# Kernel optimization log

Hardware: AMD Instinct MI355X
Metric: run time of the kernel (lower is better)

## Reference

```python
import jax, jax.numpy as jnp
import numpy as np

N, E = 50000, 800000
IN, OUT, ED = 64, 128, 16
L_CONV, CLS, L_CLS = 4, 256, 2
NUM_MOLS = 2000
BN_INV = 1.0 / np.sqrt(1.0 + 1e-5).astype(np.float32)  # BN eval: running_mean=0, running_var=1


def leaky(v):
    return jnp.where(v > 0, v, 0.01 * v)


def gine_conv(x, src, dst, edge_attr, eW, eb, W, b, gamma, beta):
    # PyG GINEConv (eps=0): nn(x + sum_j relu(x_j + lin_e(edge_attr)))
    e = edge_attr @ eW + eb                       # [E, d_in]
    msg = jax.nn.relu(x[src] + e)                 # [E, d_in]
    agg = jax.ops.segment_sum(msg, dst, num_segments=N)  # [N, d_in]
    h = (x + agg) @ W + b                         # [N, OUT]
    h = gamma * (h * BN_INV) + beta               # BatchNorm1d (eval)
    return leaky(h)                               # LeakyReLU inside nn (Dropout=identity)


def setup_inputs() -> dict:
    key = jax.random.key(0)
    ks = jax.random.split(key, 24)
    s = 0.05
    inp = {
        "x": jax.random.normal(ks[0], (N, IN), jnp.float32),
        "edge_index": jax.random.randint(ks[1], (2, E), 0, N, jnp.int32),
        "edge_attr": jax.random.normal(ks[2], (E, ED), jnp.float32),
        "batch": jnp.sort(jax.random.randint(ks[3], (N,), 0, NUM_MOLS, jnp.int32)),
        "conv1_W": jax.random.normal(ks[4], (IN, OUT), jnp.float32) * s,
        "conv1_b": jnp.zeros((OUT,), jnp.float32),
        "conv1_gamma": jnp.ones((OUT,), jnp.float32),
        "conv1_beta": jnp.zeros((OUT,), jnp.float32),
        "conv1_eW": jax.random.normal(ks[5], (ED, IN), jnp.float32) * s,
        "conv1_eb": jnp.zeros((IN,), jnp.float32),
        "conv_W": jax.random.normal(ks[6], (L_CONV, OUT, OUT), jnp.float32) * s,
        "conv_b": jnp.zeros((L_CONV, OUT), jnp.float32),
        "conv_gamma": jnp.ones((L_CONV, OUT), jnp.float32),
        "conv_beta": jnp.zeros((L_CONV, OUT), jnp.float32),
        "conv_eW": jax.random.normal(ks[7], (L_CONV, ED, OUT), jnp.float32) * s,
        "conv_eb": jnp.zeros((L_CONV, OUT), jnp.float32),
        "cls1_W": jax.random.normal(ks[8], (OUT * (L_CONV + 1), CLS), jnp.float32) * s,
        "cls1_b": jnp.zeros((CLS,), jnp.float32),
        "cls_W": jax.random.normal(ks[9], (L_CLS, CLS, CLS), jnp.float32) * s,
        "cls_b": jnp.zeros((L_CLS, CLS), jnp.float32),
        "final_W": jax.random.normal(ks[10], (CLS, 1), jnp.float32) * s,
        "final_b": jnp.zeros((1,), jnp.float32),
    }
    return inp


def reference(x, edge_index, edge_attr, batch,
              conv1_W, conv1_b, conv1_gamma, conv1_beta, conv1_eW, conv1_eb,
              conv_W, conv_b, conv_gamma, conv_beta, conv_eW, conv_eb,
              cls1_W, cls1_b, cls_W, cls_b, final_W, final_b):
    src, dst = edge_index[0], edge_index[1]
    h = gine_conv(x, src, dst, edge_attr, conv1_eW, conv1_eb,
                  conv1_W, conv1_b, conv1_gamma, conv1_beta)
    h = leaky(h)  # outer LeakyReLU in forward (note: conv1 output not in hs)
    hs = []
    for i in range(conv_W.shape[0]):
        h = gine_conv(h, src, dst, edge_attr, conv_eW[i], conv_eb[i],
                      conv_W[i], conv_b[i], conv_gamma[i], conv_beta[i])
        h = leaky(h)
        hs.append(h)
    h_pool = jax.ops.segment_sum(h, batch, num_segments=NUM_MOLS)  # global_add_pool
    h_pool_nodes = h_pool[batch]  # repeat_interleave by per-mol counts (batch sorted)
    h = jnp.concatenate(hs + [h_pool_nodes], axis=1)  # [N, OUT*(L_CONV+1)]
    h = h @ cls1_W + cls1_b  # no activation after classifier1 (as in source)
    for i in range(cls_W.shape[0]):
        h = leaky(h @ cls_W[i] + cls_b[i])
    return jax.nn.sigmoid(h @ final_W + final_b)  # [N, 1]
```

## Files before the change

### kernel.cpp

```cpp
#include <hip/hip_runtime.h>
#include <hip/hip_bf16.h>
#include <math.h>

#define N_NODES 50000
#define N_EDGES 800000
#define N_MOLS  2000
#define EPB     128

static constexpr float BN_INV_F = 0.9999950000374997f;

enum { ACT_NONE = 0, ACT_LEAKY = 1, ACT_BN_DL = 2 };

typedef float f32x4 __attribute__((ext_vector_type(4)));
typedef short bf16x8 __attribute__((ext_vector_type(8)));

static __device__ __forceinline__ float b2f(short s) {
    unsigned u = ((unsigned)(unsigned short)s) << 16;
    return __builtin_bit_cast(float, u);
}
static __device__ __forceinline__ short f2bs(float v) {
    return __builtin_bit_cast(short, __float2bfloat16(v));
}


__global__ void hist_kernel(const int* __restrict__ ei, int* __restrict__ cnt) {
    int e = blockIdx.x * 256 + threadIdx.x;
    if (e < N_EDGES) atomicAdd(&cnt[ei[N_EDGES + e]], 1);
}

__global__ __launch_bounds__(1024) void scan1_kernel(const int* __restrict__ cnt,
                                                     int* __restrict__ incl,
                                                     int* __restrict__ bsum) {
    __shared__ int sd[1024];
    int i = blockIdx.x * 1024 + threadIdx.x;
    int v = (i < N_NODES) ? cnt[i] : 0;
    sd[threadIdx.x] = v;
    __syncthreads();
    for (int off = 1; off < 1024; off <<= 1) {
        int t = (threadIdx.x >= off) ? sd[threadIdx.x - off] : 0;
        __syncthreads();
        sd[threadIdx.x] += t;
        __syncthreads();
    }
    incl[i] = sd[threadIdx.x];
    if (threadIdx.x == 1023) bsum[blockIdx.x] = sd[1023];
}

__global__ void scan2_kernel(const int* __restrict__ bsum, int* __restrict__ bex, int nblk) {
    if (threadIdx.x == 0) {
        int run = 0;
        for (int b = 0; b < nblk; ++b) { bex[b] = run; run += bsum[b]; }
    }
}

__global__ __launch_bounds__(1024) void scan3_kernel(const int* __restrict__ cnt,
                                                     const int* __restrict__ incl,
                                                     const int* __restrict__ bex,
                                                     int* __restrict__ cursor) {
    int i = blockIdx.x * 1024 + threadIdx.x;
    if (i < N_NODES) cursor[i] = bex[blockIdx.x] + incl[i] - cnt[i];
}

__global__ void scatter_kernel(const int* __restrict__ ei, int* __restrict__ cursor,
                               const float* __restrict__ ea,
                               int* __restrict__ srcs, int* __restrict__ dsts,
                               __hip_bfloat16* __restrict__ eas) {
    int e = blockIdx.x * 256 + threadIdx.x;
    if (e < N_EDGES) {
        int d = ei[N_EDGES + e];
        int pos = atomicAdd(&cursor[d], 1);
        srcs[pos] = ei[e];
        dsts[pos] = d;
        const f32x4* s4 = (const f32x4*)(ea + (size_t)e * 16);
        f32x4 a0 = s4[0], a1 = s4[1], a2 = s4[2], a3 = s4[3];
        bf16x8 lo, hi;
#pragma unroll
        for (int j = 0; j < 4; ++j) {
            lo[j] = f2bs(a0[j]); lo[4 + j] = f2bs(a1[j]);
            hi[j] = f2bs(a2[j]); hi[4 + j] = f2bs(a3[j]);
        }
        bf16x8* d8 = (bf16x8*)(eas + (size_t)pos * 16);
        d8[0] = lo; d8[1] = hi;
    }
}


__global__ __launch_bounds__(256) void cvt_all_kernel(
        const float* __restrict__ c1W, const float* __restrict__ cW,
        const float* __restrict__ cls1W, const float* __restrict__ clsW,
        const float* __restrict__ c1eW, const float* __restrict__ ceW,
        __hip_bfloat16* __restrict__ wt1, __hip_bfloat16* __restrict__ wtc,
        __hip_bfloat16* __restrict__ wtcls1, __hip_bfloat16* __restrict__ wtcls,
        __hip_bfloat16* __restrict__ ewt1, __hip_bfloat16* __restrict__ ewtc) {
    int o = blockIdx.x * 256 + threadIdx.x;
    auto cvt = [](const float* s, __hip_bfloat16* d, int K, int Nc, int off) {
        int n = off / K, k = off - n * K;
        d[off] = __float2bfloat16(s[(size_t)k * Nc + n]);
    };
    if (o < 8192) cvt(c1W, wt1, 64, 128, o);
    else if (o < 73728)  { int s = o - 8192;   int i = s >> 14, off = s & 16383;
        cvt(cW + i * 16384, wtc + i * 16384, 128, 128, off); }
    else if (o < 237568) cvt(cls1W, wtcls1, 640, 256, o - 73728);
    else if (o < 368640) { int s = o - 237568; int i = s >> 16, off = s & 65535;
        cvt(clsW + i * 65536, wtcls + i * 65536, 256, 256, off); }
    else if (o < 369664) cvt(c1eW, ewt1, 16, 64, o - 368640);
    else if (o < 377856) { int s = o - 369664; int i = s >> 11, off = s & 2047;
        cvt(ceW + i * 2048, ewtc + i * 2048, 16, 128, off); }
}


template<int D, bool F32IN>
__global__ __launch_bounds__(256) void edge_mfma_kernel(
        const void* __restrict__ hin_, int ld,
        const __hip_bfloat16* __restrict__ eas,
        const int* __restrict__ srcs,
        const int* __restrict__ dsts,
        const __hip_bfloat16* __restrict__ eWt,
        const float* __restrict__ eb,
        float* __restrict__ t32) {
    constexpr int SP = D + 4;
    constexpr int NCT = D / 16;
    constexpr int GROUPS = 256 / D;
    constexpr int EPG = EPB / GROUPS;
    __shared__ __hip_bfloat16 e_lds[EPB * SP];
    const int tid = threadIdx.x;
    const int wid = tid >> 6, lane = tid & 63;
    const int lrow = lane & 15;
    const int lkg = lane >> 4;
    const bool hiK = lkg >= 2;
    const int lko = (lkg & 1) * 8;
    const int p0 = blockIdx.x * EPB;

    bf16x8 bfrag[NCT];
#pragma unroll
    for (int ct = 0; ct < NCT; ++ct) {
        bf16x8 bv = *reinterpret_cast<const bf16x8*>(&eWt[(ct * 16 + lrow) * 16 + lko]);
        if (hiK) bv = (bf16x8){0, 0, 0, 0, 0, 0, 0, 0};
        bfrag[ct] = bv;
    }
#pragma unroll
    for (int et = 0; et < 2; ++et) {
        const int erow = (wid * 2 + et) * 16;
        bf16x8 av = *reinterpret_cast<const bf16x8*>(
            &eas[(size_t)(p0 + erow + lrow) * 16 + lko]);
        if (hiK) av = (bf16x8){0, 0, 0, 0, 0, 0, 0, 0};
        const int r0 = erow + lkg * 4;
#pragma unroll
        for (int ct = 0; ct < NCT; ++ct) {
            f32x4 c = (f32x4){0.f, 0.f, 0.f, 0.f};
            c = __builtin_amdgcn_mfma_f32_16x16x32_bf16(av, bfrag[ct], c, 0, 0, 0);
            const int col = ct * 16 + lrow;
            const float bi = eb[col];
#pragma unroll
            for (int r = 0; r < 4; ++r)
                e_lds[(r0 + r) * SP + col] = __float2bfloat16(c[r] + bi);
        }
    }
    __syncthreads();

    const float* hf = (const float*)hin_;
    const __hip_bfloat16* hb = (const __hip_bfloat16*)hin_;
    const int g = tid / D;
    const int f = tid - g * D;
    const int q0 = g * EPG;
    int cur = dsts[p0 + q0];
    float acc = 0.f;
    for (int q = q0; q < q0 + EPG; q += 8) {
        int s[8], d[8];
#pragma unroll
        for (int j = 0; j < 8; ++j) { s[j] = srcs[p0 + q + j]; d[j] = dsts[p0 + q + j]; }
        float h[8];
#pragma unroll
        for (int j = 0; j < 8; ++j)
            h[j] = F32IN ? hf[(size_t)s[j] * ld + f]
                         : __bfloat162float(hb[(size_t)s[j] * ld + f]);
        float e[8];
#pragma unroll
        for (int j = 0; j < 8; ++j)
            e[j] = __bfloat162float(e_lds[(q + j) * SP + f]);
#pragma unroll
        for (int j = 0; j < 8; ++j) {
            if (d[j] != cur) {
                atomicAdd(&t32[(size_t)cur * D + f], acc);
                acc = 0.f; cur = d[j];
            }
            acc += fmaxf(h[j] + e[j], 0.f);
        }
    }
    atomicAdd(&t32[(size_t)cur * D + f], acc);
}


template<int DIN, int DOUT, int WR, int WC, int MT, int NT, int ACT, int SELF>
__global__ __launch_bounds__(256) void mfma_lin_kernel(
        const void* __restrict__ A_, int lda,
        const float* __restrict__ t32,
        const __hip_bfloat16* __restrict__ Wt,
        const float* __restrict__ bias,
        const float* __restrict__ gamma,
        const float* __restrict__ beta,
        __hip_bfloat16* __restrict__ C, int ldc) {
    constexpr int BROWS = WR * MT * 16;
    constexpr int NKS = DIN / 32;
    static_assert(WC * NT * 16 == DOUT, "cols");
    static_assert(WR * WC == 4, "waves");
    const int wid = threadIdx.x >> 6, lane = threadIdx.x & 63;
    const int wr = wid / WC, wc = wid % WC;
    const int row_base = blockIdx.x * BROWS + wr * MT * 16;
    const int col0 = wc * NT * 16;
    const int lrow = lane & 15;
    const int lk = (lane >> 4) * 8;

    f32x4 acc[MT][NT];
#pragma unroll
    for (int i = 0; i < MT; ++i)
#pragma unroll
        for (int j = 0; j < NT; ++j) acc[i][j] = (f32x4){0.f, 0.f, 0.f, 0.f};

    for (int ks = 0; ks < NKS; ++ks) {
        const int kc = ks * 32 + lk;
        bf16x8 b[NT];
#pragma unroll
        for (int nt = 0; nt < NT; ++nt)
            b[nt] = *reinterpret_cast<const bf16x8*>(
                &Wt[(size_t)(col0 + nt * 16 + lrow) * DIN + kc]);
#pragma unroll
        for (int mt = 0; mt < MT; ++mt) {
            int arow = row_base + mt * 16 + lrow;
            arow = arow < N_NODES ? arow : N_NODES - 1;
            bf16x8 a;
            if constexpr (SELF == 0) {
                a = *reinterpret_cast<const bf16x8*>(
                    &((const __hip_bfloat16*)A_)[(size_t)arow * lda + kc]);
            } else {
                f32x4 t0 = *(const f32x4*)&t32[(size_t)arow * DIN + kc];
                f32x4 t1 = *(const f32x4*)&t32[(size_t)arow * DIN + kc + 4];
                if constexpr (SELF == 1) {
                    f32x4 h0 = *(const f32x4*)&((const float*)A_)[(size_t)arow * lda + kc];
                    f32x4 h1 = *(const f32x4*)&((const float*)A_)[(size_t)arow * lda + kc + 4];
#pragma unroll
                    for (int j = 0; j < 4; ++j) {
                        a[j]     = f2bs(t0[j] + h0[j]);
                        a[4 + j] = f2bs(t1[j] + h1[j]);
                    }
                } else {
                    bf16x8 hv = *reinterpret_cast<const bf16x8*>(
                        &((const __hip_bfloat16*)A_)[(size_t)arow * lda + kc]);
#pragma unroll
                    for (int j = 0; j < 4; ++j) {
                        a[j]     = f2bs(t0[j] + b2f(hv[j]));
                        a[4 + j] = f2bs(t1[j] + b2f(hv[4 + j]));
                    }
                }
            }
#pragma unroll
            for (int nt = 0; nt < NT; ++nt)
                acc[mt][nt] = __builtin_amdgcn_mfma_f32_16x16x32_bf16(
                    a, b[nt], acc[mt][nt], 0, 0, 0);
        }
    }

#pragma unroll
    for (int mt = 0; mt < MT; ++mt) {
        int r0 = row_base + mt * 16 + (lane >> 4) * 4;
#pragma unroll
        for (int nt = 0; nt < NT; ++nt) {
            int c = col0 + nt * 16 + lrow;
            float bi = bias[c];
            float ga = (ACT == ACT_BN_DL) ? gamma[c] : 0.f;
            float be = (ACT == ACT_BN_DL) ? beta[c] : 0.f;
#pragma unroll
            for (int r = 0; r < 4; ++r) {
                int row = r0 + r;
                if (row < N_NODES) {
                    float v = acc[mt][nt][r] + bi;
                    if (ACT == ACT_BN_DL) {
                        v = ga * (v * BN_INV_F) + be;
                        v = v > 0.f ? v : 1e-4f * v;
                    } else if (ACT == ACT_LEAKY) {
                        v = v > 0.f ? v : 0.01f * v;
                    }
                    C[(size_t)row * ldc + c] = __float2bfloat16(v);
                }
            }
        }
    }
}


__global__ void pool_add_kernel(const __hip_bfloat16* __restrict__ concat,
                                const int* __restrict__ batch,
                                float* __restrict__ pool) {
    int idx = blockIdx.x * 256 + threadIdx.x;
    if (idx >= N_NODES * 128) return;
    int n = idx >> 7, f = idx & 127;
    atomicAdd(&pool[batch[n] * 128 + f],
              __bfloat162float(concat[(size_t)n * 640 + 384 + f]));
}

__global__ void pool_gather_kernel(__hip_bfloat16* __restrict__ concat,
                                   const int* __restrict__ batch,
                                   const float* __restrict__ pool) {
    int idx = blockIdx.x * 256 + threadIdx.x;
    if (idx >= N_NODES * 128) return;
    int n = idx >> 7, f = idx & 127;
    concat[(size_t)n * 640 + 512 + f] = __float2bfloat16(pool[batch[n] * 128 + f]);
}


__global__ __launch_bounds__(256) void final_kernel(const __hip_bfloat16* __restrict__ A,
                                                    const float* __restrict__ fW,
                                                    const float* __restrict__ fb,
                                                    float* __restrict__ out) {
    int wave = threadIdx.x >> 6;
    int lane = threadIdx.x & 63;
    int row = blockIdx.x * 4 + wave;
    const __hip_bfloat16* ar = A + (size_t)row * 256;
    float p = 0.f;
#pragma unroll
    for (int i = 0; i < 4; ++i) {
        int k = lane + i * 64;
        p += __bfloat162float(ar[k]) * fW[k];
    }
#pragma unroll
    for (int off = 32; off >= 1; off >>= 1) p += __shfl_xor(p, off, 64);
    if (lane == 0) out[row] = 1.f / (1.f + expf(-(p + fb[0])));
}


extern "C" void kernel_launch(void* const* d_in, const int* in_sizes, int n_in,
                              void* d_out, int out_size, void* d_ws, size_t ws_size,
                              hipStream_t stream) {
    const float* x     = (const float*)d_in[0];
    const int*   ei    = (const int*)d_in[1];
    const float* ea    = (const float*)d_in[2];
    const int*   batch = (const int*)d_in[3];
    const float* c1W   = (const float*)d_in[4];
    const float* c1b   = (const float*)d_in[5];
    const float* c1g   = (const float*)d_in[6];
    const float* c1be  = (const float*)d_in[7];
    const float* c1eW  = (const float*)d_in[8];
    const float* c1eb  = (const float*)d_in[9];
    const float* cW    = (const float*)d_in[10];
    const float* cb    = (const float*)d_in[11];
    const float* cg    = (const float*)d_in[12];
    const float* cbe   = (const float*)d_in[13];
    const float* ceW   = (const float*)d_in[14];
    const float* ceb   = (const float*)d_in[15];
    const float* cls1W = (const float*)d_in[16];
    const float* cls1b = (const float*)d_in[17];
    const float* clsW  = (const float*)d_in[18];
    const float* clsb  = (const float*)d_in[19];
    const float* fW    = (const float*)d_in[20];
    const float* fb    = (const float*)d_in[21];
    float* out = (float*)d_out;

    char* ws = (char*)d_ws;
    size_t off = 0;
    auto alloc = [&](size_t bytes) {
        void* p = ws + off;
        off += (bytes + 255) & ~(size_t)255;
        return p;
    };
    const int NBLK = (N_NODES + 1023) / 1024;
    int*   srcs   = (int*)alloc((size_t)N_EDGES * 4);
    int*   dsts   = (int*)alloc((size_t)N_EDGES * 4);
    int*   cursor = (int*)alloc((size_t)N_NODES * 4);
    int*   cnt    = (int*)alloc((size_t)N_NODES * 4);
    int*   incl   = (int*)alloc((size_t)NBLK * 1024 * 4);
    int*   bsum   = (int*)alloc((size_t)NBLK * 4);
    int*   bex    = (int*)alloc((size_t)NBLK * 4);
    __hip_bfloat16* eas = (__hip_bfloat16*)alloc((size_t)N_EDGES * 16 * 2);
    float* t32    = (float*)alloc((size_t)N_NODES * 128 * 4);
    __hip_bfloat16* h1     = (__hip_bfloat16*)alloc((size_t)N_NODES * 128 * 2);
    float*          pool   = (float*)alloc((size_t)N_MOLS * 128 * 4);
    __hip_bfloat16* concat = (__hip_bfloat16*)alloc((size_t)N_NODES * 640 * 2);
    __hip_bfloat16* clsA   = (__hip_bfloat16*)alloc((size_t)N_NODES * 256 * 2);
    __hip_bfloat16* wt1    = (__hip_bfloat16*)alloc((size_t)128 * 64 * 2);
    __hip_bfloat16* wtc    = (__hip_bfloat16*)alloc((size_t)4 * 128 * 128 * 2);
    __hip_bfloat16* wtcls1 = (__hip_bfloat16*)alloc((size_t)256 * 640 * 2);
    __hip_bfloat16* wtcls  = (__hip_bfloat16*)alloc((size_t)2 * 256 * 256 * 2);
    __hip_bfloat16* ewt1   = (__hip_bfloat16*)alloc((size_t)64 * 16 * 2);
    __hip_bfloat16* ewtc   = (__hip_bfloat16*)alloc((size_t)4 * 128 * 16 * 2);
    __hip_bfloat16* clsB   = concat;

    hipMemsetAsync(cnt, 0, (size_t)N_NODES * 4, stream);
    hipMemsetAsync(pool, 0, (size_t)N_MOLS * 128 * 4, stream);

    hist_kernel<<<(N_EDGES + 255) / 256, 256, 0, stream>>>(ei, cnt);
    scan1_kernel<<<NBLK, 1024, 0, stream>>>(cnt, incl, bsum);
    scan2_kernel<<<1, 64, 0, stream>>>(bsum, bex, NBLK);
    scan3_kernel<<<NBLK, 1024, 0, stream>>>(cnt, incl, bex, cursor);
    scatter_kernel<<<(N_EDGES + 255) / 256, 256, 0, stream>>>(ei, cursor, ea, srcs, dsts, eas);

    cvt_all_kernel<<<(377856 + 255) / 256, 256, 0, stream>>>(
        c1W, cW, cls1W, clsW, c1eW, ceW, wt1, wtc, wtcls1, wtcls, ewt1, ewtc);

    const int NEB = N_EDGES / EPB;
    const int GRID_LIN = (N_NODES + 63) / 64;

    hipMemsetAsync(t32, 0, (size_t)N_NODES * 64 * 4, stream);
    edge_mfma_kernel<64, true><<<NEB, 256, 0, stream>>>(
        x, 64, eas, srcs, dsts, ewt1, c1eb, t32);
    mfma_lin_kernel<64, 128, 2, 2, 2, 4, ACT_BN_DL, 1><<<GRID_LIN, 256, 0, stream>>>(
        x, 64, t32, wt1, c1b, c1g, c1be, h1, 128);

    for (int i = 0; i < 4; ++i) {
        const void* hin = (i == 0) ? (const void*)h1 : (const void*)(concat + (size_t)(i - 1) * 128);
        int ld = (i == 0) ? 128 : 640;
        hipMemsetAsync(t32, 0, (size_t)N_NODES * 128 * 4, stream);
        edge_mfma_kernel<128, false><<<NEB, 256, 0, stream>>>(
            hin, ld, eas, srcs, dsts, ewtc + (size_t)i * 2048, ceb + (size_t)i * 128, t32);
        mfma_lin_kernel<128, 128, 2, 2, 2, 4, ACT_BN_DL, 2><<<GRID_LIN, 256, 0, stream>>>(
            hin, ld, t32, wtc + (size_t)i * 16384, cb + i * 128,
            cg + i * 128, cbe + i * 128, concat + (size_t)i * 128, 640);
    }

    pool_add_kernel<<<(N_NODES * 128 + 255) / 256, 256, 0, stream>>>(concat, batch, pool);
    pool_gather_kernel<<<(N_NODES * 128 + 255) / 256, 256, 0, stream>>>(concat, batch, pool);

    mfma_lin_kernel<640, 256, 1, 4, 4, 4, ACT_NONE, 0><<<GRID_LIN, 256, 0, stream>>>(
        concat, 640, nullptr, wtcls1, cls1b, nullptr, nullptr, clsA, 256);
    mfma_lin_kernel<256, 256, 1, 4, 4, 4, ACT_LEAKY, 0><<<GRID_LIN, 256, 0, stream>>>(
        clsA, 256, nullptr, wtcls, clsb, nullptr, nullptr, clsB, 256);
    mfma_lin_kernel<256, 256, 1, 4, 4, 4, ACT_LEAKY, 0><<<GRID_LIN, 256, 0, stream>>>(
        clsB, 256, nullptr, wtcls + 256 * 256, clsb + 256, nullptr, nullptr, clsA, 256);
    final_kernel<<<N_NODES / 4, 256, 0, stream>>>(clsA, fW, fb, out);
}
```

Before: 934.7 us.

## Restructure MFMA linear kernel to preload A rows and use 32-row blocks

The linear kernel now uses a fixed 2x2 wave layout where each wave owns one 16-row tile, and each block covers 32 rows instead of 64, which doubles the grid. The wave's full A row strip across all K steps is loaded into registers up front, and the B fragments are then streamed inside the MFMA loop. The aim is more parallelism and better overlap of the A loads. The cost is less reuse of each weight fragment, since every wave now reloads B for only one M tile. For the DIN=640 classifier layer, holding 20 A fragments per lane raises register pressure.

```diff
diff --git a/kernel.cpp b/kernel.cpp
--- a/kernel.cpp
+++ b/kernel.cpp
@@ -191,7 +191,7 @@
 }
 
 
-template<int DIN, int DOUT, int WR, int WC, int MT, int NT, int ACT, int SELF>
+template<int DIN, int DOUT, int ACT, int SELF>
 __global__ __launch_bounds__(256) void mfma_lin_kernel(
         const void* __restrict__ A_, int lda,
         const float* __restrict__ t32,
@@ -200,88 +200,95 @@
         const float* __restrict__ gamma,
         const float* __restrict__ beta,
         __hip_bfloat16* __restrict__ C, int ldc) {
-    constexpr int BROWS = WR * MT * 16;
+    constexpr int NT = DOUT / 32;
     constexpr int NKS = DIN / 32;
-    static_assert(WC * NT * 16 == DOUT, "cols");
-    static_assert(WR * WC == 4, "waves");
     const int wid = threadIdx.x >> 6, lane = threadIdx.x & 63;
-    const int wr = wid / WC, wc = wid % WC;
-    const int row_base = blockIdx.x * BROWS + wr * MT * 16;
-    const int col0 = wc * NT * 16;
+    const int wr = wid >> 1, wc = wid & 1;
+    const int row_base = blockIdx.x * 32 + wr * 16;
+    const int col_base = wc * NT * 16;
     const int lrow = lane & 15;
     const int lk = (lane >> 4) * 8;
 
-    f32x4 acc[MT][NT];
-#pragma unroll
-    for (int i = 0; i < MT; ++i)
-#pragma unroll
-        for (int j = 0; j < NT; ++j) acc[i][j] = (f32x4){0.f, 0.f, 0.f, 0.f};
-
+    int arow = row_base + lrow;
+    arow = arow < N_NODES ? arow : N_NODES - 1;
+
+    bf16x8 a[NKS];
+    if constexpr (SELF == 0) {
+        const __hip_bfloat16* Ab = (const __hip_bfloat16*)A_;
+#pragma unroll
+        for (int ks = 0; ks < NKS; ++ks)
+            a[ks] = *reinterpret_cast<const bf16x8*>(&Ab[(size_t)arow * lda + ks * 32 + lk]);
+    } else if constexpr (SELF == 1) {
+        const float* Af = (const float*)A_;
+        f32x4 t0[NKS], t1[NKS], h0[NKS], h1[NKS];
+#pragma unroll
+        for (int ks = 0; ks < NKS; ++ks) {
+            const int kc = ks * 32 + lk;
+            t0[ks] = *(const f32x4*)&t32[(size_t)arow * DIN + kc];
+            t1[ks] = *(const f32x4*)&t32[(size_t)arow * DIN + kc + 4];
+            h0[ks] = *(const f32x4*)&Af[(size_t)arow * lda + kc];
+            h1[ks] = *(const f32x4*)&Af[(size_t)arow * lda + kc + 4];
+        }
+#pragma unroll
+        for (int ks = 0; ks < NKS; ++ks)
+#pragma unroll
+            for (int j = 0; j < 4; ++j) {
+                a[ks][j]     = f2bs(t0[ks][j] + h0[ks][j]);
+                a[ks][4 + j] = f2bs(t1[ks][j] + h1[ks][j]);
+            }
+    } else {
+        const __hip_bfloat16* Ab = (const __hip_bfloat16*)A_;
+        f32x4 t0[NKS], t1[NKS];
+        bf16x8 hv[NKS];
+#pragma unroll
+        for (int ks = 0; ks < NKS; ++ks) {
+            const int kc = ks * 32 + lk;
+            t0[ks] = *(const f32x4*)&t32[(size_t)arow * DIN + kc];
+            t1[ks] = *(const f32x4*)&t32[(size_t)arow * DIN + kc + 4];
+            hv[ks] = *reinterpret_cast<const bf16x8*>(&Ab[(size_t)arow * lda + kc]);
+        }
+#pragma unroll
+        for (int ks = 0; ks < NKS; ++ks)
+#pragma unroll
+            for (int j = 0; j < 4; ++j) {
+                a[ks][j]     = f2bs(t0[ks][j] + b2f(hv[ks][j]));
+                a[ks][4 + j] = f2bs(t1[ks][j] + b2f(hv[ks][4 + j]));
+            }
+    }
+
+    f32x4 acc[NT];
+#pragma unroll
+    for (int nt = 0; nt < NT; ++nt) acc[nt] = (f32x4){0.f, 0.f, 0.f, 0.f};
+#pragma unroll
     for (int ks = 0; ks < NKS; ++ks) {
         const int kc = ks * 32 + lk;
-        bf16x8 b[NT];
-#pragma unroll
-        for (int nt = 0; nt < NT; ++nt)
-            b[nt] = *reinterpret_cast<const bf16x8*>(
-                &Wt[(size_t)(col0 + nt * 16 + lrow) * DIN + kc]);
-#pragma unroll
-        for (int mt = 0; mt < MT; ++mt) {
-            int arow = row_base + mt * 16 + lrow;
-            arow = arow < N_NODES ? arow : N_NODES - 1;
-            bf16x8 a;
-            if constexpr (SELF == 0) {
-                a = *reinterpret_cast<const bf16x8*>(
-                    &((const __hip_bfloat16*)A_)[(size_t)arow * lda + kc]);
-            } else {
-                f32x4 t0 = *(const f32x4*)&t32[(size_t)arow * DIN + kc];
-                f32x4 t1 = *(const f32x4*)&t32[(size_t)arow * DIN + kc + 4];
-                if constexpr (SELF == 1) {
-                    f32x4 h0 = *(const f32x4*)&((const float*)A_)[(size_t)arow * lda + kc];
-                    f32x4 h1 = *(const f32x4*)&((const float*)A_)[(size_t)arow * lda + kc + 4];
-#pragma unroll
-                    for (int j = 0; j < 4; ++j) {
-                        a[j]     = f2bs(t0[j] + h0[j]);
-                        a[4 + j] = f2bs(t1[j] + h1[j]);
-                    }
-                } else {
-                    bf16x8 hv = *reinterpret_cast<const bf16x8*>(
-                        &((const __hip_bfloat16*)A_)[(size_t)arow * lda + kc]);
-#pragma unroll
-                    for (int j = 0; j < 4; ++j) {
-                        a[j]     = f2bs(t0[j] + b2f(hv[j]));
-                        a[4 + j] = f2bs(t1[j] + b2f(hv[4 + j]));
-                    }
+#pragma unroll
+        for (int nt = 0; nt < NT; ++nt) {
+            bf16x8 b = *reinterpret_cast<const bf16x8*>(
+                &Wt[(size_t)(col_base + nt * 16 + lrow) * DIN + kc]);
+            acc[nt] = __builtin_amdgcn_mfma_f32_16x16x32_bf16(a[ks], b, acc[nt], 0, 0, 0);
+        }
+    }
+
+    const int r0 = row_base + (lane >> 4) * 4;
+#pragma unroll
+    for (int nt = 0; nt < NT; ++nt) {
+        int c = col_base + nt * 16 + lrow;
+        float bi = bias[c];
+        float ga = (ACT == ACT_BN_DL) ? gamma[c] : 0.f;
+        float be = (ACT == ACT_BN_DL) ? beta[c] : 0.f;
+#pragma unroll
+        for (int r = 0; r < 4; ++r) {
+            int row = r0 + r;
+            if (row < N_NODES) {
+                float v = acc[nt][r] + bi;
+                if (ACT == ACT_BN_DL) {
+                    v = ga * (v * BN_INV_F) + be;
+                    v = v > 0.f ? v : 1e-4f * v;
+                } else if (ACT == ACT_LEAKY) {
+                    v = v > 0.f ? v : 0.01f * v;
                 }
-            }
-#pragma unroll
-            for (int nt = 0; nt < NT; ++nt)
-                acc[mt][nt] = __builtin_amdgcn_mfma_f32_16x16x32_bf16(
-                    a, b[nt], acc[mt][nt], 0, 0, 0);
-        }
-    }
-
-#pragma unroll
-    for (int mt = 0; mt < MT; ++mt) {
-        int r0 = row_base + mt * 16 + (lane >> 4) * 4;
-#pragma unroll
-        for (int nt = 0; nt < NT; ++nt) {
-            int c = col0 + nt * 16 + lrow;
-            float bi = bias[c];
-            float ga = (ACT == ACT_BN_DL) ? gamma[c] : 0.f;
-            float be = (ACT == ACT_BN_DL) ? beta[c] : 0.f;
-#pragma unroll
-            for (int r = 0; r < 4; ++r) {
-                int row = r0 + r;
-                if (row < N_NODES) {
-                    float v = acc[mt][nt][r] + bi;
-                    if (ACT == ACT_BN_DL) {
-                        v = ga * (v * BN_INV_F) + be;
-                        v = v > 0.f ? v : 1e-4f * v;
-                    } else if (ACT == ACT_LEAKY) {
-                        v = v > 0.f ? v : 0.01f * v;
-                    }
-                    C[(size_t)row * ldc + c] = __float2bfloat16(v);
-                }
+                C[(size_t)row * ldc + c] = __float2bfloat16(v);
             }
         }
     }
@@ -397,12 +404,12 @@
         c1W, cW, cls1W, clsW, c1eW, ceW, wt1, wtc, wtcls1, wtcls, ewt1, ewtc);
 
     const int NEB = N_EDGES / EPB;
-    const int GRID_LIN = (N_NODES + 63) / 64;
+    const int GRID_LIN = (N_NODES + 31) / 32;
 
     hipMemsetAsync(t32, 0, (size_t)N_NODES * 64 * 4, stream);
     edge_mfma_kernel<64, true><<<NEB, 256, 0, stream>>>(
         x, 64, eas, srcs, dsts, ewt1, c1eb, t32);
-    mfma_lin_kernel<64, 128, 2, 2, 2, 4, ACT_BN_DL, 1><<<GRID_LIN, 256, 0, stream>>>(
+    mfma_lin_kernel<64, 128, ACT_BN_DL, 1><<<GRID_LIN, 256, 0, stream>>>(
         x, 64, t32, wt1, c1b, c1g, c1be, h1, 128);
 
     for (int i = 0; i < 4; ++i) {
@@ -411,7 +418,7 @@
         hipMemsetAsync(t32, 0, (size_t)N_NODES * 128 * 4, stream);
         edge_mfma_kernel<128, false><<<NEB, 256, 0, stream>>>(
             hin, ld, eas, srcs, dsts, ewtc + (size_t)i * 2048, ceb + (size_t)i * 128, t32);
-        mfma_lin_kernel<128, 128, 2, 2, 2, 4, ACT_BN_DL, 2><<<GRID_LIN, 256, 0, stream>>>(
+        mfma_lin_kernel<128, 128, ACT_BN_DL, 2><<<GRID_LIN, 256, 0, stream>>>(
             hin, ld, t32, wtc + (size_t)i * 16384, cb + i * 128,
             cg + i * 128, cbe + i * 128, concat + (size_t)i * 128, 640);
     }
@@ -419,11 +426,11 @@
     pool_add_kernel<<<(N_NODES * 128 + 255) / 256, 256, 0, stream>>>(concat, batch, pool);
     pool_gather_kernel<<<(N_NODES * 128 + 255) / 256, 256, 0, stream>>>(concat, batch, pool);
 
-    mfma_lin_kernel<640, 256, 1, 4, 4, 4, ACT_NONE, 0><<<GRID_LIN, 256, 0, stream>>>(
+    mfma_lin_kernel<640, 256, ACT_NONE, 0><<<GRID_LIN, 256, 0, stream>>>(
         concat, 640, nullptr, wtcls1, cls1b, nullptr, nullptr, clsA, 256);
-    mfma_lin_kernel<256, 256, 1, 4, 4, 4, ACT_LEAKY, 0><<<GRID_LIN, 256, 0, stream>>>(
+    mfma_lin_kernel<256, 256, ACT_LEAKY, 0><<<GRID_LIN, 256, 0, stream>>>(
         clsA, 256, nullptr, wtcls, clsb, nullptr, nullptr, clsB, 256);
-    mfma_lin_kernel<256, 256, 1, 4, 4, 4, ACT_LEAKY, 0><<<GRID_LIN, 256, 0, stream>>>(
+    mfma_lin_kernel<256, 256, ACT_LEAKY, 0><<<GRID_LIN, 256, 0, stream>>>(
         clsB, 256, nullptr, wtcls + 256 * 256, clsb + 256, nullptr, nullptr, clsA, 256);
     final_kernel<<<N_NODES / 4, 256, 0, stream>>>(clsA, fW, fb, out);
 }
```

Result: slower. 1.068 ms (+14.3%).
